# Kernel tuning notes

Measured on AMD Instinct MI355X. Metric: run time of the kernel, lower is better.

Reference implementation:

```python
import jax, jax.numpy as jnp
import numpy as np

N = 50000
E = 800000
F_IN = 128
HEADS = 4
OUT_PER_HEAD = 32  # out_features 128 / 4 heads
NEG_SLOPE = 0.2


def setup_inputs() -> dict:
    key = jax.random.key(0)
    k1, k2, k3, k4, k5 = jax.random.split(key, 5)
    x = jax.random.normal(k1, (N, F_IN), dtype=jnp.float32)
    edge_index = jax.random.randint(k2, (2, E), 0, N, dtype=jnp.int64)
    # xavier-uniform style init
    limW = float(np.sqrt(6.0 / (F_IN + OUT_PER_HEAD)))
    W = jax.random.uniform(k3, (HEADS, F_IN, OUT_PER_HEAD), jnp.float32, -limW, limW)
    lima = float(np.sqrt(6.0 / (OUT_PER_HEAD + 1)))
    a_l = jax.random.uniform(k4, (HEADS, OUT_PER_HEAD), jnp.float32, -lima, lima)
    a_r = jax.random.uniform(k5, (HEADS, OUT_PER_HEAD), jnp.float32, -lima, lima)
    return {"x": x, "edge_index": edge_index, "W": W, "a_l": a_l, "a_r": a_r}


def _leaky_relu(v, slope):
    return jnp.where(v >= 0, v, slope * v)


def reference(x, edge_index, W, a_l, a_r):
    src, dst = edge_index[0], edge_index[1]
    n = x.shape[0]
    # Wh: [heads, N, out_per_head]
    Wh = jnp.einsum('nf,kfh->knh', x, W)
    e_l = jnp.einsum('knh,kh->kn', Wh, a_l)  # [heads, N]
    e_r = jnp.einsum('knh,kh->kn', Wh, a_r)
    # per-edge attention logits [heads, E]
    e = _leaky_relu(e_l[:, src] + e_r[:, dst], NEG_SLOPE)
    # segment softmax over incoming edges of each dst node
    seg_max = jax.vmap(lambda ee: jax.ops.segment_max(ee, dst, num_segments=n))(e)
    seg_max = jnp.maximum(seg_max, -1e9)  # torch init value for empty nodes
    exp_e = jnp.exp(e - seg_max[:, dst])
    denom = jax.vmap(lambda ee: jax.ops.segment_sum(ee, dst, num_segments=n))(exp_e)
    alpha = exp_e / (denom[:, dst] + 1e-16)  # [heads, E]
    # weighted aggregation: [heads, E, out_per_head] scattered into [heads, N, out_per_head]
    weighted = alpha[..., None] * Wh[:, src, :]
    out = jax.vmap(lambda w: jax.ops.segment_sum(w, dst, num_segments=n))(weighted)
    # concat heads -> [N, heads*out_per_head]
    return out.transpose(1, 0, 2).reshape(n, -1)
```

## Files before the change

kernel.cpp:

```cpp
#include <hip/hip_runtime.h>

#define NN 50000
#define NE 800000
#define FIN 128
#define NH 4
#define OPH 32
#define FOUT 128
#define NSLOPE 0.2f
#define NGB ((NN + 63) / 64)
#define BCOLS 144
#define LDA 136
#define BSH 5
#define BUKSZ 32
#define NBUK ((NN + BUKSZ - 1) >> BSH)
#define SUBCH 4096
#define NPSUB ((NE + SUBCH - 1) / SUBCH)
#define NSC ((NPSUB + 3) / 4)
#define SLOTQ 15
#define SLOTS 64
#define GRID1 (5 * NPSUB)

typedef __attribute__((ext_vector_type(8))) short short8v;
typedef __attribute__((ext_vector_type(4))) float f32x4;

static __device__ __forceinline__ unsigned short f2bf(float f) {
  unsigned int u = __float_as_uint(f);
  u += 0x7fffu + ((u >> 16) & 1u);
  return (unsigned short)(u >> 16);
}

__global__ __launch_bounds__(128) void k_prep(
    const float* __restrict__ W, const float* __restrict__ a_l,
    const float* __restrict__ a_r, unsigned short* __restrict__ Btf) {
  const int c = blockIdx.x;
  const int f = threadIdx.x;
  unsigned short v = 0;
  if (c < 128) {
    const int h = c >> 5, o = c & 31;
    v = f2bf(W[h * (FIN * OPH) + f * OPH + o]);
  } else if (c < 136) {
    const int j = c - 128;
    const int h = j & 3;
    const float* __restrict__ av = (j < 4) ? a_l : a_r;
    float s = 0.f;
    for (int o = 0; o < 32; ++o)
      s += W[h * (FIN * OPH) + f * OPH + o] * av[h * OPH + o];
    v = f2bf(s);
  }
  const int ct = c >> 4, lr = c & 15;
  const int s = f >> 5, rem = f & 31, lk = rem >> 3, j = rem & 7;
  const int l = lr + 16 * lk;
  Btf[(((size_t)ct * 4 + s) * 64 + l) * 8 + j] = v;
}

__global__ __launch_bounds__(256) void k_gemm_part(
    const float* __restrict__ x, const unsigned short* __restrict__ Btf,
    const int* __restrict__ src, const int* __restrict__ dst,
    unsigned int* __restrict__ ebuf,
    unsigned short* __restrict__ WhU, float* __restrict__ e_l4,
    float* __restrict__ e_r4) {
  __shared__ union U {
    unsigned short As[64 * LDA];
    int cntl[NBUK];
  } sh;
  const int t = threadIdx.x;
  const int bid = blockIdx.x;

  if (bid % 5 == 4) {
    const int pidx = bid / 5;
    const int sc = pidx >> 2;
    const int sub = pidx & 3;
    const int base = pidx * SUBCH;
    for (int b = t; b < NBUK; b += 256) sh.cntl[b] = 0;
    __syncthreads();
    unsigned int* __restrict__ myreg =
        ebuf + (size_t)sc * NBUK * 64 + sub * 16;
#pragma unroll
    for (int k = 0; k < SUBCH / 256; ++k) {
      const int i = base + k * 256 + t;
      if (i < NE) {
        const int d = dst[i];
        const int b = d >> BSH;
        const int lp = atomicAdd(&sh.cntl[b], 1);
        if (lp < SLOTQ)
          myreg[(size_t)b * 64 + 1 + lp] =
              ((unsigned int)(d & (BUKSZ - 1)) << 16) | (unsigned int)src[i];
      }
    }
    __syncthreads();
    for (int b = t; b < NBUK; b += 256)
      myreg[(size_t)b * 64] = (unsigned int)min(sh.cntl[b], SLOTQ);
    return;
  }

  const int g = bid - bid / 5;
  if (g >= NGB) return;
  const int m0 = g * 64;

#pragma unroll
  for (int i = 0; i < 8; ++i) {
    const int fidx = t + i * 256;
    const int node = fidx >> 5;
    const int fg = fidx & 31;
    const int n = m0 + node;
    float4 v = make_float4(0.f, 0.f, 0.f, 0.f);
    if (n < NN) v = *(const float4*)(x + (size_t)n * FIN + fg * 4);
    ushort4 pk;
    pk.x = f2bf(v.x); pk.y = f2bf(v.y); pk.z = f2bf(v.z); pk.w = f2bf(v.w);
    *(ushort4*)&sh.As[node * LDA + fg * 4] = pk;
  }
  __syncthreads();

  const int w = t >> 6;
  const int l = t & 63;
  const int lr = l & 15;
  const int lk = l >> 4;

  short8v a_frag[4];
#pragma unroll
  for (int kk = 0; kk < 4; ++kk)
    a_frag[kk] = *(const short8v*)&sh.As[(w * 16 + lr) * LDA + kk * 32 + lk * 8];

  f32x4 acc[9];
#pragma unroll
  for (int ct = 0; ct < 9; ++ct) acc[ct] = (f32x4){0.f, 0.f, 0.f, 0.f};

#pragma unroll
  for (int ct = 0; ct < 9; ++ct) {
    const unsigned short* __restrict__ Bp = Btf + ((size_t)ct * 4) * 512 + l * 8;
    short8v b0 = *(const short8v*)(Bp);
    short8v b1 = *(const short8v*)(Bp + 512);
    short8v b2 = *(const short8v*)(Bp + 1024);
    short8v b3 = *(const short8v*)(Bp + 1536);
    acc[ct] = __builtin_amdgcn_mfma_f32_16x16x32_bf16(a_frag[0], b0, acc[ct], 0, 0, 0);
    acc[ct] = __builtin_amdgcn_mfma_f32_16x16x32_bf16(a_frag[1], b1, acc[ct], 0, 0, 0);
    acc[ct] = __builtin_amdgcn_mfma_f32_16x16x32_bf16(a_frag[2], b2, acc[ct], 0, 0, 0);
    acc[ct] = __builtin_amdgcn_mfma_f32_16x16x32_bf16(a_frag[3], b3, acc[ct], 0, 0, 0);
  }

#pragma unroll
  for (int ct = 0; ct < 9; ++ct) {
#pragma unroll
    for (int reg = 0; reg < 4; ++reg) {
      const int n = m0 + w * 16 + lk * 4 + reg;
      if (n >= NN) continue;
      const float v = acc[ct][reg];
      if (ct < 8) {
        WhU[(size_t)n * FOUT + ct * 16 + lr] = f2bf(v);
      } else if (lr < 4) {
        e_l4[n * NH + lr] = v;
      } else if (lr < 8) {
        e_r4[n * NH + (lr - 4)] = v;
      }
    }
  }
}

__global__ __launch_bounds__(256) void k_lists_agg(
    const unsigned int* __restrict__ ebuf,
    const float* __restrict__ e_l4, const float* __restrict__ e_r4,
    const unsigned int* __restrict__ Whh, float* __restrict__ out) {
  __shared__ int lists[BUKSZ][SLOTS];
  __shared__ int cur[BUKSZ];
  __shared__ float exs[4][64][4];

  const int b = blockIdx.x;
  const int t = threadIdx.x;
  const int w = t >> 6;
  const int lane = t & 63;

  if (t < BUKSZ) cur[t] = 0;
  __syncthreads();

  const int word = lane & 15;
#pragma unroll
  for (int it = 0; it < (NPSUB + 15) / 16; ++it) {
    const int j = it * 16 + w * 4 + (lane >> 4);
    unsigned int v = 0;
    if (j < NPSUB) {
      const int sc = j >> 2, sub = j & 3;
      v = ebuf[(size_t)sc * NBUK * 64 + (size_t)b * 64 + sub * 16 + word];
    }
    const unsigned int cnt = __shfl(v, lane & 48);
    if (j < NPSUB && word >= 1 && word <= (int)cnt) {
      const int idx = (int)(v >> 16);
      const int lp = atomicAdd(&cur[idx], 1);
      if (lp < SLOTS) lists[idx][lp] = (int)(v & 0xFFFFu);
    }
  }
  __syncthreads();

  const int h = lane >> 4;
#pragma unroll
  for (int nl = 0; nl < 8; ++nl) {
    const int idx = w * 8 + nl;
    const int n = (b << BSH) + idx;
    if (n >= NN) continue;
    const int deg = min(cur[idx], SLOTS);
    const float4 ern = *(const float4*)&e_r4[n * NH];

    float e0 = 0.f, e1 = 0.f, e2 = 0.f, e3 = 0.f;
    if (lane < deg) {
      const int s = lists[idx][lane];
      const float4 el = *(const float4*)&e_l4[s * NH];
      float l0 = el.x + ern.x; l0 = (l0 >= 0.f) ? l0 : NSLOPE * l0;
      float l1 = el.y + ern.y; l1 = (l1 >= 0.f) ? l1 : NSLOPE * l1;
      float l2 = el.z + ern.z; l2 = (l2 >= 0.f) ? l2 : NSLOPE * l2;
      float l3 = el.w + ern.w; l3 = (l3 >= 0.f) ? l3 : NSLOPE * l3;
      e0 = __expf(l0); e1 = __expf(l1);
      e2 = __expf(l2); e3 = __expf(l3);
    }
    *(float4*)exs[w][lane] = make_float4(e0, e1, e2, e3);

    float acc0 = 0.f, acc1 = 0.f, den = 0.f;
    int jl = 0;
    for (; jl + 7 < deg; jl += 8) {
      int sj[8];
#pragma unroll
      for (int u = 0; u < 8; ++u) sj[u] = lists[idx][jl + u];
      unsigned int vv[8];
#pragma unroll
      for (int u = 0; u < 8; ++u) vv[u] = Whh[(size_t)sj[u] * 64 + lane];
#pragma unroll
      for (int u = 0; u < 8; ++u) {
        const float wH = exs[w][jl + u][h];
        den += wH;
        acc0 = fmaf(wH, __uint_as_float(vv[u] << 16), acc0);
        acc1 = fmaf(wH, __uint_as_float(vv[u] & 0xffff0000u), acc1);
      }
    }
    for (; jl < deg; ++jl) {
      const int sj = lists[idx][jl];
      const float wH = exs[w][jl][h];
      const unsigned int v = Whh[(size_t)sj * 64 + lane];
      den += wH;
      acc0 = fmaf(wH, __uint_as_float(v << 16), acc0);
      acc1 = fmaf(wH, __uint_as_float(v & 0xffff0000u), acc1);
    }

    const float inv = 1.f / (den + 1e-16f);
    *(float2*)&out[(size_t)n * FOUT + 2 * lane] =
        make_float2(acc0 * inv, acc1 * inv);
  }
}

extern "C" void kernel_launch(void* const* d_in, const int* in_sizes, int n_in,
                              void* d_out, int out_size, void* d_ws, size_t ws_size,
                              hipStream_t stream) {
  const float* x   = (const float*)d_in[0];
  const int*   ei  = (const int*)d_in[1];
  const float* W   = (const float*)d_in[2];
  const float* a_l = (const float*)d_in[3];
  const float* a_r = (const float*)d_in[4];
  float* out = (float*)d_out;

  const int* src = ei;
  const int* dst = ei + NE;

  unsigned int* Whh = (unsigned int*)d_ws;
  float* e_l4     = (float*)(Whh + (size_t)NN * 64);
  float* e_r4     = e_l4 + NN * NH;
  unsigned short* Btf = (unsigned short*)(e_r4 + NN * NH);
  unsigned int* ebuf = (unsigned int*)(Btf + 9 * 4 * 64 * 8);
  (void)ws_size; (void)in_sizes; (void)n_in; (void)out_size;

  k_prep<<<BCOLS, 128, 0, stream>>>(W, a_l, a_r, Btf);

  k_gemm_part<<<GRID1, 256, 0, stream>>>(
      x, Btf, src, dst, ebuf, (unsigned short*)Whh, e_l4, e_r4);

  k_lists_agg<<<NBUK, 256, 0, stream>>>(ebuf, e_l4, e_r4, Whh, out);
}
```

Baseline: 70.02 us.

## Split list building and aggregation into separate kernels with one node per wave

The fused bucket kernel, which built per-node adjacency lists and then aggregated eight nodes per wave in sequence, is split into two kernels. A list kernel writes 16-bit neighbor lists and degrees to global memory, and a new aggregation kernel assigns one destination node per wavefront across NN/4 blocks. The aim is much more parallelism and latency hiding during the gather-bound aggregation. The cost is an extra launch plus a global round-trip for the lists (about 6.4MB written and read back).

```diff
diff --git a/kernel.cpp b/kernel.cpp
--- a/kernel.cpp
+++ b/kernel.cpp
@@ -156,13 +156,11 @@
   }
 }
 
-__global__ __launch_bounds__(256) void k_lists_agg(
+__global__ __launch_bounds__(256) void k_lists(
     const unsigned int* __restrict__ ebuf,
-    const float* __restrict__ e_l4, const float* __restrict__ e_r4,
-    const unsigned int* __restrict__ Whh, float* __restrict__ out) {
-  __shared__ int lists[BUKSZ][SLOTS];
+    unsigned short* __restrict__ lists_g, int* __restrict__ degs) {
+  __shared__ __align__(16) unsigned short lists[BUKSZ][SLOTS];
   __shared__ int cur[BUKSZ];
-  __shared__ float exs[4][64][4];
 
   const int b = blockIdx.x;
   const int t = threadIdx.x;
@@ -185,63 +183,81 @@
     if (j < NPSUB && word >= 1 && word <= (int)cnt) {
       const int idx = (int)(v >> 16);
       const int lp = atomicAdd(&cur[idx], 1);
-      if (lp < SLOTS) lists[idx][lp] = (int)(v & 0xFFFFu);
+      if (lp < SLOTS) lists[idx][lp] = (unsigned short)(v & 0xFFFFu);
     }
   }
   __syncthreads();
 
+  const int idx = t >> 3, ch = t & 7;
+  const int node = b * BUKSZ + idx;
+  if (node < NN) {
+    const uint4 pk = *(const uint4*)&lists[idx][ch * 8];
+    *(uint4*)&lists_g[(size_t)node * SLOTS + ch * 8] = pk;
+  }
+  if (t < BUKSZ && b * BUKSZ + t < NN)
+    degs[b * BUKSZ + t] = min(cur[t], SLOTS);
+}
+
+__global__ __launch_bounds__(256) void k_agg(
+    const int* __restrict__ degs, const unsigned short* __restrict__ lists_g,
+    const float* __restrict__ e_l4, const float* __restrict__ e_r4,
+    const unsigned int* __restrict__ Whh, float* __restrict__ out) {
+  __shared__ unsigned short ls[4][64];
+  __shared__ float exs[4][64][4];
+
+  const int t = threadIdx.x;
+  const int w = t >> 6;
+  const int lane = t & 63;
+  const int n = blockIdx.x * 4 + w;
+
+  const int deg = min(degs[n], SLOTS);
+  const float4 ern = *(const float4*)&e_r4[n * NH];
+  const unsigned short s16 = lists_g[(size_t)n * SLOTS + lane];
+  ls[w][lane] = s16;
+
+  float e0 = 0.f, e1 = 0.f, e2 = 0.f, e3 = 0.f;
+  if (lane < deg) {
+    const int s = (int)s16;
+    const float4 el = *(const float4*)&e_l4[s * NH];
+    float l0 = el.x + ern.x; l0 = (l0 >= 0.f) ? l0 : NSLOPE * l0;
+    float l1 = el.y + ern.y; l1 = (l1 >= 0.f) ? l1 : NSLOPE * l1;
+    float l2 = el.z + ern.z; l2 = (l2 >= 0.f) ? l2 : NSLOPE * l2;
+    float l3 = el.w + ern.w; l3 = (l3 >= 0.f) ? l3 : NSLOPE * l3;
+    e0 = __expf(l0); e1 = __expf(l1);
+    e2 = __expf(l2); e3 = __expf(l3);
+  }
+  *(float4*)exs[w][lane] = make_float4(e0, e1, e2, e3);
+
   const int h = lane >> 4;
-#pragma unroll
-  for (int nl = 0; nl < 8; ++nl) {
-    const int idx = w * 8 + nl;
-    const int n = (b << BSH) + idx;
-    if (n >= NN) continue;
-    const int deg = min(cur[idx], SLOTS);
-    const float4 ern = *(const float4*)&e_r4[n * NH];
-
-    float e0 = 0.f, e1 = 0.f, e2 = 0.f, e3 = 0.f;
-    if (lane < deg) {
-      const int s = lists[idx][lane];
-      const float4 el = *(const float4*)&e_l4[s * NH];
-      float l0 = el.x + ern.x; l0 = (l0 >= 0.f) ? l0 : NSLOPE * l0;
-      float l1 = el.y + ern.y; l1 = (l1 >= 0.f) ? l1 : NSLOPE * l1;
-      float l2 = el.z + ern.z; l2 = (l2 >= 0.f) ? l2 : NSLOPE * l2;
-      float l3 = el.w + ern.w; l3 = (l3 >= 0.f) ? l3 : NSLOPE * l3;
-      e0 = __expf(l0); e1 = __expf(l1);
-      e2 = __expf(l2); e3 = __expf(l3);
-    }
-    *(float4*)exs[w][lane] = make_float4(e0, e1, e2, e3);
-
-    float acc0 = 0.f, acc1 = 0.f, den = 0.f;
-    int jl = 0;
-    for (; jl + 7 < deg; jl += 8) {
-      int sj[8];
-#pragma unroll
-      for (int u = 0; u < 8; ++u) sj[u] = lists[idx][jl + u];
-      unsigned int vv[8];
-#pragma unroll
-      for (int u = 0; u < 8; ++u) vv[u] = Whh[(size_t)sj[u] * 64 + lane];
-#pragma unroll
-      for (int u = 0; u < 8; ++u) {
-        const float wH = exs[w][jl + u][h];
-        den += wH;
-        acc0 = fmaf(wH, __uint_as_float(vv[u] << 16), acc0);
-        acc1 = fmaf(wH, __uint_as_float(vv[u] & 0xffff0000u), acc1);
-      }
-    }
-    for (; jl < deg; ++jl) {
-      const int sj = lists[idx][jl];
-      const float wH = exs[w][jl][h];
-      const unsigned int v = Whh[(size_t)sj * 64 + lane];
+  float acc0 = 0.f, acc1 = 0.f, den = 0.f;
+  int jl = 0;
+  for (; jl + 7 < deg; jl += 8) {
+    int sj[8];
+#pragma unroll
+    for (int u = 0; u < 8; ++u) sj[u] = ls[w][jl + u];
+    unsigned int vv[8];
+#pragma unroll
+    for (int u = 0; u < 8; ++u) vv[u] = Whh[(size_t)sj[u] * 64 + lane];
+#pragma unroll
+    for (int u = 0; u < 8; ++u) {
+      const float wH = exs[w][jl + u][h];
       den += wH;
-      acc0 = fmaf(wH, __uint_as_float(v << 16), acc0);
-      acc1 = fmaf(wH, __uint_as_float(v & 0xffff0000u), acc1);
-    }
-
-    const float inv = 1.f / (den + 1e-16f);
-    *(float2*)&out[(size_t)n * FOUT + 2 * lane] =
-        make_float2(acc0 * inv, acc1 * inv);
-  }
+      acc0 = fmaf(wH, __uint_as_float(vv[u] << 16), acc0);
+      acc1 = fmaf(wH, __uint_as_float(vv[u] & 0xffff0000u), acc1);
+    }
+  }
+  for (; jl < deg; ++jl) {
+    const int sj = ls[w][jl];
+    const float wH = exs[w][jl][h];
+    const unsigned int v = Whh[(size_t)sj * 64 + lane];
+    den += wH;
+    acc0 = fmaf(wH, __uint_as_float(v << 16), acc0);
+    acc1 = fmaf(wH, __uint_as_float(v & 0xffff0000u), acc1);
+  }
+
+  const float inv = 1.f / (den + 1e-16f);
+  *(float2*)&out[(size_t)n * FOUT + 2 * lane] =
+      make_float2(acc0 * inv, acc1 * inv);
 }
 
 extern "C" void kernel_launch(void* const* d_in, const int* in_sizes, int n_in,
@@ -262,6 +278,8 @@
   float* e_r4     = e_l4 + NN * NH;
   unsigned short* Btf = (unsigned short*)(e_r4 + NN * NH);
   unsigned int* ebuf = (unsigned int*)(Btf + 9 * 4 * 64 * 8);
+  unsigned short* lists_g = (unsigned short*)(ebuf + (size_t)NSC * NBUK * 64);
+  int* degs = (int*)(lists_g + (size_t)NN * SLOTS);
   (void)ws_size; (void)in_sizes; (void)n_in; (void)out_size;
 
   k_prep<<<BCOLS, 128, 0, stream>>>(W, a_l, a_r, Btf);
@@ -269,5 +287,7 @@
   k_gemm_part<<<GRID1, 256, 0, stream>>>(
       x, Btf, src, dst, ebuf, (unsigned short*)Whh, e_l4, e_r4);
 
-  k_lists_agg<<<NBUK, 256, 0, stream>>>(ebuf, e_l4, e_r4, Whh, out);
-}
+  k_lists<<<NBUK, 256, 0, stream>>>(ebuf, lists_g, degs);
+
+  k_agg<<<NN / 4, 256, 0, stream>>>(degs, lists_g, e_l4, e_r4, Whh, out);
+}
```

Result: no change. 69.87 us (-0.2%).
